# Performance work log

Measured on AMD Instinct MI355X. Metric: run time of the kernel, lower is better.

## Reference

```python
import jax, jax.numpy as jnp
import numpy as np

B, S, D = 4, 2048, 1024
H, DH = 16, 64  # dim_q = dim_k = D // H
DFF = 4096


def setup_inputs() -> dict:
    key = jax.random.key(0)
    ks = jax.random.split(key, 12)
    sd = 0.02
    x = jax.random.normal(ks[0], (B, S, D), dtype=jnp.float32)
    mask = jax.random.randint(ks[1], (B, S, S), 0, 2) == 1  # True = masked
    Wq = jax.random.normal(ks[2], (H, D, DH), dtype=jnp.float32) * sd
    bq = jnp.zeros((H, DH), dtype=jnp.float32)
    Wk = jax.random.normal(ks[3], (H, D, DH), dtype=jnp.float32) * sd
    bk = jnp.zeros((H, DH), dtype=jnp.float32)
    Wv = jax.random.normal(ks[4], (H, D, DH), dtype=jnp.float32) * sd
    bv = jnp.zeros((H, DH), dtype=jnp.float32)
    Wo = jax.random.normal(ks[5], (H * DH, D), dtype=jnp.float32) * sd
    bo = jnp.zeros((D,), dtype=jnp.float32)
    W1 = jax.random.normal(ks[6], (D, DFF), dtype=jnp.float32) * sd
    b1 = jnp.zeros((DFF,), dtype=jnp.float32)
    W2 = jax.random.normal(ks[7], (DFF, D), dtype=jnp.float32) * sd
    b2 = jnp.zeros((D,), dtype=jnp.float32)
    return dict(x=x, mask=mask, Wq=Wq, bq=bq, Wk=Wk, bk=bk, Wv=Wv, bv=bv,
                Wo=Wo, bo=bo, W1=W1, b1=b1, W2=W2, b2=b2)


def reference(x, mask, Wq, bq, Wk, bk, Wv, bv, Wo, bo, W1, b1, W2, b2):
    # x: [B,S,D]; mask: [B,S,S] bool (True -> masked)
    # Per-head projections, batched over heads: [B,H,S,DH]
    q = jnp.einsum('bsd,hde->bhse', x, Wq) + bq[None, :, None, :]
    k = jnp.einsum('bsd,hde->bhse', x, Wk) + bk[None, :, None, :]
    v = jnp.einsum('bsd,hde->bhse', x, Wv) + bv[None, :, None, :]
    # NOTE: source scales by sqrt(seq_len) (query.size(1)), reproduced faithfully.
    scale = x.shape[1] ** 0.5
    scores = jnp.einsum('bhse,bhte->bhst', q, k) / scale  # [B,H,S,S]
    scores = jnp.where(mask[:, None, :, :], -1e9, scores)
    attn = jax.nn.softmax(scores, axis=-1)
    ctx = jnp.einsum('bhst,bhte->bhse', attn, v)  # [B,H,S,DH]
    # concat heads -> [B,S,H*DH], output projection
    ctx = jnp.transpose(ctx, (0, 2, 1, 3)).reshape(x.shape[0], x.shape[1], -1)
    out = ctx @ Wo + bo
    # FFN (no residual/LayerNorm in source; dropout = identity in eval)
    h = jax.nn.relu(out @ W1 + b1)
    return h @ W2 + b2
```

## Files before the change

kernel.cpp:

```cpp
#include <hip/hip_runtime.h>
#include <hip/hip_bf16.h>


#define SDIM 2048
#define DDIM 1024

using floatx4 = __attribute__((ext_vector_type(4))) float;
using bf16x8  = __attribute__((ext_vector_type(8))) __bf16;
using bf16x4  = __attribute__((ext_vector_type(4))) __bf16;
using short4v = __attribute__((ext_vector_type(4))) short;

#define GLDS16(gptr, lptr)                                                        \
    __builtin_amdgcn_global_load_lds(                                             \
        (const __attribute__((address_space(1))) void*)(uintptr_t)(gptr),         \
        (__attribute__((address_space(3))) void*)(uintptr_t)(lptr), 16, 0, 0)


__global__ void k_f2b(const float* __restrict__ in, __bf16* __restrict__ out) {
    long i = ((long)blockIdx.x * 256 + threadIdx.x) * 4;
    float4 f = *(const float4*)(in + i);
    bf16x4 v;
    v[0] = (__bf16)f.x; v[1] = (__bf16)f.y; v[2] = (__bf16)f.z; v[3] = (__bf16)f.w;
    *(bf16x4*)(out + i) = v;
}

__global__ void k_tr(const float* __restrict__ in, __bf16* __restrict__ out, int R, int C) {
    __shared__ float t[32][33];
    int nrt = R >> 5;
    int tr = blockIdx.x % nrt, tc = blockIdx.x / nrt;
    int r0 = tr * 32, c0 = tc * 32;
    int lx = threadIdx.x & 31, ly = threadIdx.x >> 5;
    #pragma unroll
    for (int i = 0; i < 32; i += 8) t[ly + i][lx] = in[(long)(r0 + ly + i) * C + c0 + lx];
    __syncthreads();
    #pragma unroll
    for (int i = 0; i < 32; i += 8) out[(long)(c0 + ly + i) * R + r0 + lx] = (__bf16)t[lx][ly + i];
}

__global__ void k_pack_qkvw(const float* __restrict__ Wq, const float* __restrict__ Wk,
                            const float* __restrict__ Wv, __bf16* __restrict__ out) {
    int bid = blockIdx.x;
    int dht = bid & 1;
    int dt = (bid >> 1) & 31;
    int h = (bid >> 6) & 15;
    int which = bid >> 10;
    const float* W = (which == 0) ? Wq : (which == 1) ? Wk : Wv;
    __shared__ float t[32][33];
    int lx = threadIdx.x & 31, ly = threadIdx.x >> 5;
    const float* src = W + ((long)h * 1024 + dt * 32) * 64 + dht * 32;
    #pragma unroll
    for (int i = 0; i < 32; i += 8) t[ly + i][lx] = src[(ly + i) * 64 + lx];
    __syncthreads();
    __bf16* dst = out + ((long)(which * 1024 + h * 64 + dht * 32)) * 1024 + dt * 32;
    #pragma unroll
    for (int i = 0; i < 32; i += 8) dst[(long)(ly + i) * 1024 + lx] = (__bf16)t[lx][ly + i];
}

__global__ void k_pack_qkvb(const float* bq, const float* bk, const float* bv, float* out) {
    int i = blockIdx.x * 256 + threadIdx.x;
    if (i < 3072) {
        int which = i >> 10, r = i & 1023;
        const float* s = (which == 0) ? bq : (which == 1) ? bk : bv;
        out[i] = s[r];
    }
}

__global__ void k_probe(const unsigned* __restrict__ m, int* flag) {
    __shared__ int bad;
    if (threadIdx.x == 0) bad = 0;
    __syncthreads();
    int local = 0;
    for (int i = 0; i < 64; i++) {
        unsigned w = m[threadIdx.x + 256 * i];
        if (w != 0u && w != 1u && w != 0x3f800000u) local = 1;
    }
    if (local) atomicOr(&bad, 1);
    __syncthreads();
    if (threadIdx.x == 0) *flag = bad ? 0 : 1;
}

__global__ void k_pack_mask(const void* __restrict__ mask, const int* __restrict__ flag,
                            unsigned long long* __restrict__ bits) {
    long wid = ((long)blockIdx.x * 256 + threadIdx.x) >> 6;
    int lane = threadIdx.x & 63;
    long e = wid * 64 + lane;
    bool pred;
    if (*flag) pred = ((const unsigned*)mask)[e] != 0u;
    else       pred = ((const unsigned char*)mask)[e] != 0;
    unsigned long long bal = __ballot(pred);
    if (lane == 0) bits[wid] = bal;
}

__global__ void k_trv(const __bf16* __restrict__ Vrow, __bf16* __restrict__ Vt) {
    __shared__ __bf16 t[32][72];
    int p = blockIdx.x >> 6, ts = blockIdx.x & 63;
    int tid = threadIdx.x;
    const __bf16* src = Vrow + ((long)p * 2048 + ts * 32) * 64;
    int s = tid >> 3, c = (tid & 7) * 8;
    *(bf16x8*)&t[s][c] = *(const bf16x8*)&src[s * 64 + c];
    __syncthreads();
    int dh = tid >> 2, sb = (tid & 3) * 8;
    bf16x8 w;
    #pragma unroll
    for (int j = 0; j < 8; j++) w[j] = t[sb + j][dh];
    *(bf16x8*)&Vt[((long)p * 64 + dh) * 2048 + ts * 32 + sb] = w;
}

#define QSZ 8388608L

template <int MODE>
__global__ __launch_bounds__(256, 3) void k_gemm(const __bf16* __restrict__ A,
                                                 const __bf16* __restrict__ Bt,
                                                 const float* __restrict__ bias,
                                                 void* __restrict__ Cout, int Ndim, int K) {
    __shared__ __align__(16) __bf16 As[128 * 32];
    __shared__ __align__(16) __bf16 Bs[128 * 32];
    const int tid = threadIdx.x;
    const int wave = tid >> 6, lane = tid & 63;
    const int q = lane >> 4, l16 = lane & 15;
    const int wr = wave >> 1, wc = wave & 1;
    const long bm = (long)blockIdx.x * 128;
    const long bn = (long)blockIdx.y * 128;
    floatx4 acc[4][4] = {};

    const int srow = (lane >> 2);
    const int scol = (lane & 3) * 8;

    for (int k0 = 0; k0 < K; k0 += 32) {
        __syncthreads();
        #pragma unroll
        for (int i = 0; i < 2; i++) {
            int row = wave * 16 + i * 64 + srow;
            GLDS16(&A[(bm + row) * K + k0 + scol], (char*)As + wave * 1024 + i * 4096);
            GLDS16(&Bt[(bn + row) * K + k0 + scol], (char*)Bs + wave * 1024 + i * 4096);
        }
        __syncthreads();
        bf16x8 af[4], bfr[4];
        #pragma unroll
        for (int i = 0; i < 4; i++) af[i] = *(const bf16x8*)&As[(wr * 64 + i * 16 + l16) * 32 + q * 8];
        #pragma unroll
        for (int j = 0; j < 4; j++) bfr[j] = *(const bf16x8*)&Bs[(wc * 64 + j * 16 + l16) * 32 + q * 8];
        #pragma unroll
        for (int i = 0; i < 4; i++)
            #pragma unroll
            for (int j = 0; j < 4; j++)
                acc[i][j] = __builtin_amdgcn_mfma_f32_16x16x32_bf16(af[i], bfr[j], acc[i][j], 0, 0, 0);
    }

    const int mrow0 = (int)bm + wr * 64 + q * 4;
    const int ncol0 = (int)bn + wc * 64;
    #pragma unroll
    for (int j = 0; j < 4; j++) {
        int nbase = ncol0 + j * 16 + l16;
        float bv = bias[nbase];
        #pragma unroll
        for (int i = 0; i < 4; i++) {
            #pragma unroll
            for (int r = 0; r < 4; r++) {
                int mm = mrow0 + i * 16 + r;
                float v = acc[i][j][r] + bv;
                if (MODE == 2) v = fmaxf(v, 0.f);
                if (MODE == 3) {
                    ((float*)Cout)[(long)mm * Ndim + nbase] = v;
                } else if (MODE == 0) {
                    int which = nbase >> 10, rem = nbase & 1023;
                    int hh = rem >> 6, dh = rem & 63;
                    int bb = mm >> 11, ss = mm & 2047;
                    long pr = (long)(bb * 16 + hh);
                    __bf16* o = (__bf16*)Cout;
                    if (which == 0) {
                        v *= 0.03188152837f;
                        o[(pr * 2048 + ss) * 64 + dh] = (__bf16)v;
                    } else if (which == 1) o[QSZ + (pr * 2048 + ss) * 64 + dh] = (__bf16)v;
                    else o[3 * QSZ + (pr * 2048 + ss) * 64 + dh] = (__bf16)v;
                } else {
                    ((__bf16*)Cout)[(long)mm * Ndim + nbase] = (__bf16)v;
                }
            }
        }
    }
}

__global__ __launch_bounds__(256, 3) void k_attn(const __bf16* __restrict__ Q,
                                                 const __bf16* __restrict__ Kb,
                                                 const __bf16* __restrict__ Vt,
                                                 const unsigned* __restrict__ bitw,
                                                 __bf16* __restrict__ ctx) {
    __shared__ __align__(16) __bf16 Qs[64][72];
    __shared__ __align__(16) __bf16 Ks[128][72];
    __shared__ __align__(16) __bf16 Vts[64][136];
    __shared__ unsigned Ms[64][4];
    const int tid = threadIdx.x, wave = tid >> 6, lane = tid & 63;
    const int q = lane >> 4, l16 = lane & 15;
    const int pair = blockIdx.x & 63, qt = blockIdx.x >> 6;
    const int b = pair >> 4, h = pair & 15;

    const __bf16* Qp = Q + ((long)pair * SDIM + qt * 64) * 64;
    #pragma unroll
    for (int i = 0; i < 2; i++) {
        int v = tid + i * 256;
        int r = v >> 3, c = (v & 7) * 8;
        *(bf16x8*)&Qs[r][c] = *(const bf16x8*)&Qp[r * 64 + c];
    }
    __syncthreads();
    const bf16x8 qf0 = *(const bf16x8*)&Qs[wave * 16 + l16][q * 8];
    const bf16x8 qf1 = *(const bf16x8*)&Qs[wave * 16 + l16][32 + q * 8];

    float lacc = 0.f;
    floatx4 o[4] = {};

    const long mrow0 = (long)b * SDIM + qt * 64;

    for (int kt = 0; kt < 16; kt++) {
        __syncthreads();
        const __bf16* Kp = Kb + ((long)pair * SDIM + kt * 128) * 64;
        #pragma unroll
        for (int i = 0; i < 4; i++) {
            int v = tid + i * 256;
            int r = v >> 3, c = (v & 7) * 8;
            *(bf16x8*)&Ks[r][c] = *(const bf16x8*)&Kp[r * 64 + c];
        }
        const __bf16* Vp = Vt + (long)pair * 64 * SDIM + kt * 128;
        #pragma unroll
        for (int i = 0; i < 4; i++) {
            int v = tid + i * 256;
            int r = v >> 4, c = (v & 15) * 8;
            *(bf16x8*)&Vts[r][c] = *(const bf16x8*)&Vp[(long)r * SDIM + c];
        }
        {
            int mr = tid >> 2, mw = tid & 3;
            Ms[mr][mw] = bitw[((mrow0 + mr) << 6) + kt * 4 + mw];
        }
        __syncthreads();

        floatx4 st[8];
        #pragma unroll
        for (int ct = 0; ct < 8; ct++) {
            bf16x8 kf0 = *(const bf16x8*)&Ks[ct * 16 + l16][q * 8];
            bf16x8 kf1 = *(const bf16x8*)&Ks[ct * 16 + l16][32 + q * 8];
            floatx4 z = {};
            z = __builtin_amdgcn_mfma_f32_16x16x32_bf16(kf0, qf0, z, 0, 0, 0);
            z = __builtin_amdgcn_mfma_f32_16x16x32_bf16(kf1, qf1, z, 0, 0, 0);
            st[ct] = z;
        }
        const int lr = wave * 16 + l16;
        unsigned w0 = Ms[lr][0], w1 = Ms[lr][1], w2 = Ms[lr][2], w3 = Ms[lr][3];
        unsigned mwv[4] = {w0, w1, w2, w3};
        #pragma unroll
        for (int ct = 0; ct < 8; ct++) {
            unsigned wd = mwv[ct >> 1];
            int bp = ((ct & 1) << 4) + q * 4;
            #pragma unroll
            for (int r = 0; r < 4; r++) {
                float p = exp2f(st[ct][r]);
                p = ((wd >> (bp + r)) & 1u) ? 0.f : p;
                st[ct][r] = p;
                lacc += p;
            }
        }
        #pragma unroll
        for (int ct = 0; ct < 8; ct++) {
            union { bf16x4 b; short4v s; } pu;
            #pragma unroll
            for (int r = 0; r < 4; r++) pu.b[r] = (__bf16)st[ct][r];
            #pragma unroll
            for (int d = 0; d < 4; d++) {
                union { bf16x4 b; short4v s; } vu;
                vu.b = *(const bf16x4*)&Vts[d * 16 + l16][ct * 16 + q * 4];
                o[d] = __builtin_amdgcn_mfma_f32_16x16x16bf16_1k(vu.s, pu.s, o[d], 0, 0, 0);
            }
        }
    }
    lacc += __shfl_xor(lacc, 16);
    lacc += __shfl_xor(lacc, 32);
    float inv = 1.0f / lacc;
    int rowg = qt * 64 + wave * 16 + l16;
    long base = ((long)b * SDIM + rowg) * DDIM + h * 64;
    #pragma unroll
    for (int d = 0; d < 4; d++) {
        bf16x4 w;
        #pragma unroll
        for (int r = 0; r < 4; r++) w[r] = (__bf16)(o[d][r] * inv);
        *(bf16x4*)&ctx[base + d * 16 + q * 4] = w;
    }
}


extern "C" void kernel_launch(void* const* d_in, const int* in_sizes, int n_in,
                              void* d_out, int out_size, void* d_ws, size_t ws_size,
                              hipStream_t stream) {
    const float* x = (const float*)d_in[0];
    const void* mask = d_in[1];
    const float* Wq = (const float*)d_in[2];
    const float* bq = (const float*)d_in[3];
    const float* Wk = (const float*)d_in[4];
    const float* bk = (const float*)d_in[5];
    const float* Wv = (const float*)d_in[6];
    const float* bv = (const float*)d_in[7];
    const float* Wo = (const float*)d_in[8];
    const float* bo = (const float*)d_in[9];
    const float* W1 = (const float*)d_in[10];
    const float* b1 = (const float*)d_in[11];
    const float* W2 = (const float*)d_in[12];
    const float* b2 = (const float*)d_in[13];

    char* ws = (char*)d_ws;
    __bf16* xb   = (__bf16*)(ws + 0);
    __bf16* Qb   = (__bf16*)(ws + 16777216);
    __bf16* Kb   = (__bf16*)(ws + 33554432);
    __bf16* Vtb  = (__bf16*)(ws + 50331648);
    __bf16* Vrow = (__bf16*)(ws + 67108864);
    __bf16* hbuf = (__bf16*)(ws + 33554432);
    __bf16* wqkvt = (__bf16*)(ws + 100663296);
    __bf16* wot  = (__bf16*)(ws + 106954752);
    __bf16* w1t  = (__bf16*)(ws + 109051904);
    __bf16* w2t  = (__bf16*)(ws + 117440512);
    float* bqkv  = (float*)(ws + 125829120);
    int* flag    = (int*)(ws + 125841408);
    __bf16* ctx = xb;
    __bf16* attn_out = Qb;
    unsigned long long* bits = (unsigned long long*)wqkvt;
    (void)Vrow;

    k_f2b<<<8192, 256, 0, stream>>>(x, xb);
    k_pack_qkvw<<<3072, 256, 0, stream>>>(Wq, Wk, Wv, wqkvt);
    k_pack_qkvb<<<12, 256, 0, stream>>>(bq, bk, bv, bqkv);
    k_tr<<<1024, 256, 0, stream>>>(Wo, wot, 1024, 1024);
    k_tr<<<4096, 256, 0, stream>>>(W1, w1t, 1024, 4096);
    k_tr<<<4096, 256, 0, stream>>>(W2, w2t, 4096, 1024);
    k_probe<<<1, 256, 0, stream>>>((const unsigned*)mask, flag);

    {
        dim3 g(64, 24);
        k_gemm<0><<<g, 256, 0, stream>>>(xb, wqkvt, bqkv, (void*)Qb, 3072, 1024);
    }
    k_trv<<<4096, 256, 0, stream>>>(Vrow, Vtb);
    k_pack_mask<<<65536, 256, 0, stream>>>(mask, flag, bits);
    k_attn<<<2048, 256, 0, stream>>>(Qb, Kb, Vtb, (const unsigned*)bits, ctx);
    {
        dim3 g(64, 8);
        k_gemm<1><<<g, 256, 0, stream>>>(ctx, wot, bo, (void*)attn_out, 1024, 1024);
    }
    {
        dim3 g(64, 32);
        k_gemm<2><<<g, 256, 0, stream>>>(attn_out, w1t, b1, (void*)hbuf, 4096, 1024);
    }
    {
        dim3 g(64, 8);
        k_gemm<3><<<g, 256, 0, stream>>>(hbuf, w2t, b2, d_out, 1024, 4096);
    }
}
```

Baseline: 723.8 us.

## Use swizzled direct-to-LDS loads with BK=64 in GEMM and attention

The GEMM doubles its K tile to 64 and stages A/B through global_load_lds into an XOR-style rotated (swizzled) LDS layout, which halves the number of barriers per K. The attention kernel replaces register-staged Q/K/V copies with direct-to-LDS loads into swizzled unpadded tiles. It also reads mask words straight from global into registers instead of through LDS, and raises the occupancy hint to 4 blocks. The aim is to cut LDS bank conflicts, staging instructions and sync overhead. The risks are swizzle index errors and higher LDS use per GEMM block.

```diff
diff --git a/kernel.cpp b/kernel.cpp
--- a/kernel.cpp
+++ b/kernel.cpp
@@ -113,8 +113,8 @@
                                                  const __bf16* __restrict__ Bt,
                                                  const float* __restrict__ bias,
                                                  void* __restrict__ Cout, int Ndim, int K) {
-    __shared__ __align__(16) __bf16 As[128 * 32];
-    __shared__ __align__(16) __bf16 Bs[128 * 32];
+    __shared__ __align__(16) __bf16 As[128 * 64];
+    __shared__ __align__(16) __bf16 Bs[128 * 64];
     const int tid = threadIdx.x;
     const int wave = tid >> 6, lane = tid & 63;
     const int q = lane >> 4, l16 = lane & 15;
@@ -123,28 +123,34 @@
     const long bn = (long)blockIdx.y * 128;
     floatx4 acc[4][4] = {};
 
-    const int srow = (lane >> 2);
-    const int scol = (lane & 3) * 8;
-
-    for (int k0 = 0; k0 < K; k0 += 32) {
+    const int srow = lane >> 3;
+    const int scol = (((lane & 7) - srow) & 7) * 8;
+    const int r8 = l16 & 7;
+
+    for (int k0 = 0; k0 < K; k0 += 64) {
         __syncthreads();
         #pragma unroll
-        for (int i = 0; i < 2; i++) {
-            int row = wave * 16 + i * 64 + srow;
-            GLDS16(&A[(bm + row) * K + k0 + scol], (char*)As + wave * 1024 + i * 4096);
-            GLDS16(&Bt[(bn + row) * K + k0 + scol], (char*)Bs + wave * 1024 + i * 4096);
+        for (int c = 0; c < 4; c++) {
+            int row0 = wave * 32 + c * 8;
+            GLDS16(&A[(bm + row0 + srow) * K + k0 + scol], (char*)As + row0 * 128);
+            GLDS16(&Bt[(bn + row0 + srow) * K + k0 + scol], (char*)Bs + row0 * 128);
         }
         __syncthreads();
-        bf16x8 af[4], bfr[4];
-        #pragma unroll
-        for (int i = 0; i < 4; i++) af[i] = *(const bf16x8*)&As[(wr * 64 + i * 16 + l16) * 32 + q * 8];
-        #pragma unroll
-        for (int j = 0; j < 4; j++) bfr[j] = *(const bf16x8*)&Bs[(wc * 64 + j * 16 + l16) * 32 + q * 8];
-        #pragma unroll
-        for (int i = 0; i < 4; i++)
+        #pragma unroll
+        for (int s = 0; s < 2; s++) {
+            bf16x8 af[4], bfr[4];
+            #pragma unroll
+            for (int i = 0; i < 4; i++)
+                af[i] = *(const bf16x8*)&As[(wr * 64 + i * 16 + l16) * 64 + ((s * 4 + q + r8) & 7) * 8];
             #pragma unroll
             for (int j = 0; j < 4; j++)
-                acc[i][j] = __builtin_amdgcn_mfma_f32_16x16x32_bf16(af[i], bfr[j], acc[i][j], 0, 0, 0);
+                bfr[j] = *(const bf16x8*)&Bs[(wc * 64 + j * 16 + l16) * 64 + ((s * 4 + q + r8) & 7) * 8];
+            #pragma unroll
+            for (int i = 0; i < 4; i++)
+                #pragma unroll
+                for (int j = 0; j < 4; j++)
+                    acc[i][j] = __builtin_amdgcn_mfma_f32_16x16x32_bf16(af[i], bfr[j], acc[i][j], 0, 0, 0);
+        }
     }
 
     const int mrow0 = (int)bm + wr * 64 + q * 4;
@@ -181,71 +187,68 @@
     }
 }
 
-__global__ __launch_bounds__(256, 3) void k_attn(const __bf16* __restrict__ Q,
+__global__ __launch_bounds__(256, 4) void k_attn(const __bf16* __restrict__ Q,
                                                  const __bf16* __restrict__ Kb,
                                                  const __bf16* __restrict__ Vt,
                                                  const unsigned* __restrict__ bitw,
                                                  __bf16* __restrict__ ctx) {
-    __shared__ __align__(16) __bf16 Qs[64][72];
-    __shared__ __align__(16) __bf16 Ks[128][72];
-    __shared__ __align__(16) __bf16 Vts[64][136];
-    __shared__ unsigned Ms[64][4];
+    __shared__ __align__(16) __bf16 Qs[64 * 64];
+    __shared__ __align__(16) __bf16 Ks[128 * 64];
+    __shared__ __align__(16) __bf16 Vts[64 * 128];
     const int tid = threadIdx.x, wave = tid >> 6, lane = tid & 63;
     const int q = lane >> 4, l16 = lane & 15;
     const int pair = blockIdx.x & 63, qt = blockIdx.x >> 6;
     const int b = pair >> 4, h = pair & 15;
 
+    const int srow8 = lane >> 3;
+    const int scol8 = (((lane & 7) - srow8) & 7) * 8;
+    const int r8 = l16 & 7;
+    const int vrow = lane >> 4;
+    const int vl = lane & 15;
+
     const __bf16* Qp = Q + ((long)pair * SDIM + qt * 64) * 64;
     #pragma unroll
-    for (int i = 0; i < 2; i++) {
-        int v = tid + i * 256;
-        int r = v >> 3, c = (v & 7) * 8;
-        *(bf16x8*)&Qs[r][c] = *(const bf16x8*)&Qp[r * 64 + c];
-    }
-    __syncthreads();
-    const bf16x8 qf0 = *(const bf16x8*)&Qs[wave * 16 + l16][q * 8];
-    const bf16x8 qf1 = *(const bf16x8*)&Qs[wave * 16 + l16][32 + q * 8];
+    for (int c = 0; c < 2; c++) {
+        int row0 = wave * 16 + c * 8;
+        GLDS16(&Qp[(row0 + srow8) * 64 + scol8], (char*)Qs + row0 * 128);
+    }
+    __syncthreads();
+    const bf16x8 qf0 = *(const bf16x8*)&Qs[(wave * 16 + l16) * 64 + ((q + r8) & 7) * 8];
+    const bf16x8 qf1 = *(const bf16x8*)&Qs[(wave * 16 + l16) * 64 + ((q + 4 + r8) & 7) * 8];
 
     float lacc = 0.f;
     floatx4 o[4] = {};
-
     const long mrow0 = (long)b * SDIM + qt * 64;
 
     for (int kt = 0; kt < 16; kt++) {
         __syncthreads();
         const __bf16* Kp = Kb + ((long)pair * SDIM + kt * 128) * 64;
         #pragma unroll
-        for (int i = 0; i < 4; i++) {
-            int v = tid + i * 256;
-            int r = v >> 3, c = (v & 7) * 8;
-            *(bf16x8*)&Ks[r][c] = *(const bf16x8*)&Kp[r * 64 + c];
-        }
-        const __bf16* Vp = Vt + (long)pair * 64 * SDIM + kt * 128;
-        #pragma unroll
-        for (int i = 0; i < 4; i++) {
-            int v = tid + i * 256;
-            int r = v >> 4, c = (v & 15) * 8;
-            *(bf16x8*)&Vts[r][c] = *(const bf16x8*)&Vp[(long)r * SDIM + c];
-        }
-        {
-            int mr = tid >> 2, mw = tid & 3;
-            Ms[mr][mw] = bitw[((mrow0 + mr) << 6) + kt * 4 + mw];
-        }
+        for (int c = 0; c < 4; c++) {
+            int row0 = wave * 32 + c * 8;
+            GLDS16(&Kp[(row0 + srow8) * 64 + scol8], (char*)Ks + row0 * 128);
+        }
+        const __bf16* Vp = Vt + ((long)pair * 64) * SDIM + kt * 128;
+        #pragma unroll
+        for (int c = 0; c < 4; c++) {
+            int row0 = wave * 16 + c * 4;
+            int gsrc = ((vl - (c * 4 + vrow)) & 15) * 8;
+            GLDS16(&Vp[(long)(row0 + vrow) * SDIM + gsrc], (char*)Vts + row0 * 256);
+        }
+        const uint4 mq = *(const uint4*)(bitw + ((mrow0 + wave * 16 + l16) << 6) + kt * 4);
         __syncthreads();
 
         floatx4 st[8];
         #pragma unroll
         for (int ct = 0; ct < 8; ct++) {
-            bf16x8 kf0 = *(const bf16x8*)&Ks[ct * 16 + l16][q * 8];
-            bf16x8 kf1 = *(const bf16x8*)&Ks[ct * 16 + l16][32 + q * 8];
+            bf16x8 kf0 = *(const bf16x8*)&Ks[(ct * 16 + l16) * 64 + ((q + r8) & 7) * 8];
+            bf16x8 kf1 = *(const bf16x8*)&Ks[(ct * 16 + l16) * 64 + ((q + 4 + r8) & 7) * 8];
             floatx4 z = {};
             z = __builtin_amdgcn_mfma_f32_16x16x32_bf16(kf0, qf0, z, 0, 0, 0);
             z = __builtin_amdgcn_mfma_f32_16x16x32_bf16(kf1, qf1, z, 0, 0, 0);
             st[ct] = z;
         }
-        const int lr = wave * 16 + l16;
-        unsigned w0 = Ms[lr][0], w1 = Ms[lr][1], w2 = Ms[lr][2], w3 = Ms[lr][3];
-        unsigned mwv[4] = {w0, w1, w2, w3};
+        unsigned mwv[4] = {mq.x, mq.y, mq.z, mq.w};
         #pragma unroll
         for (int ct = 0; ct < 8; ct++) {
             unsigned wd = mwv[ct >> 1];
@@ -265,8 +268,9 @@
             for (int r = 0; r < 4; r++) pu.b[r] = (__bf16)st[ct][r];
             #pragma unroll
             for (int d = 0; d < 4; d++) {
+                int vg = (ct * 2 + (q >> 1) + l16) & 15;
                 union { bf16x4 b; short4v s; } vu;
-                vu.b = *(const bf16x4*)&Vts[d * 16 + l16][ct * 16 + q * 4];
+                vu.b = *(const bf16x4*)((const char*)Vts + (d * 16 + l16) * 256 + vg * 16 + (q & 1) * 8);
                 o[d] = __builtin_amdgcn_mfma_f32_16x16x16bf16_1k(vu.s, pu.s, o[d], 0, 0, 0);
             }
         }
```

New measurement: 634.8 us. -12.3%, faster.
